# Kernel tuning notes

Hardware: AMD Instinct MI355X
Metric: run time of the kernel (lower is better)

The kernel has to match this reference:

```python
import jax, jax.numpy as jnp
import numpy as np

EPS = 1e-12
NEG_INF = -1e30

def _slog(x):
    return jnp.log(jnp.clip(x, EPS))

def setup_inputs() -> dict:
    M, Z = 24, 1024
    key = jax.random.key(0)
    ks = jax.random.split(key, 20)
    u = lambda k, sh, s=1.0: jax.random.uniform(k, sh, dtype=jnp.float32) * s
    demin = u(ks[0], (M, M), 0.2)
    demax = demin + u(ks[1], (M, M), 1.0)
    Kn = (jax.random.uniform(ks[2], (M, M)) > 0.5).astype(jnp.float32)
    # a couple of sectors with no substitution choices (rows stay all-ones in S)
    Kn = Kn.at[0].set(0.0).at[5].set(0.0)
    housing_mask = jnp.zeros((M,), dtype=bool).at[jnp.array([M - 2, M - 1])].set(True)
    genflux_mask = (jax.random.uniform(ks[3], (M,)) > 0.2)
    return {
        'h': jnp.zeros((M, Z), jnp.float32),
        'price': u(ks[4], (M, Z)),
        't_nij': u(ks[5], (M, Z, Z)),
        'demin': demin,
        'demax': demax,
        'delta': u(ks[6], (M, M), 0.2),
        'omega': u(ks[7], (M, M)),
        'sigma': u(ks[8], (M,), 0.5),
        'Kn': Kn,
        'attractor': u(ks[9], (M, Z)) + 0.1,
        'beta': u(ks[10], (M,), 0.5),
        'lamda': u(ks[11], (M,)),
        'A_ni': u(ks[12], (M, Z)) + 0.1,
        'exog_demand': u(ks[13], (M, Z)),
        'exog_prod': u(ks[14], (M, Z)),
        'X_0': u(ks[15], (M, Z)) + 0.1,
        'X_target': u(ks[16], (M, Z)),
        'housing_mask': housing_mask,
        'genflux_mask': genflux_mask,
    }

def reference(h, price, t_nij, demin, demax, delta, omega, sigma, Kn,
              attractor, beta, lamda, A_ni, exog_demand, exog_prod,
              X_0, X_target, housing_mask, genflux_mask):
    M, Z = price.shape
    ph = price + h                                            # [n,i] prices + shadow prices
    # LocationProbability: U_nij = lamda_n*ph[n,j] + t_nij; Pr = softmax_j for genflux non-housing, else eye
    U_nij = lamda[:, None, None] * ph[:, None, :] + t_nij     # [n,i,j]
    loc_logits = _slog(A_ni)[:, None, :] - beta[:, None, None] * U_nij
    Pr_soft = jax.nn.softmax(loc_logits, axis=-1)
    loc_mask = genflux_mask & (~housing_mask)                 # sectors with location choice
    eye = jnp.eye(Z, dtype=price.dtype)
    Pr = jnp.where(loc_mask[:, None, None], Pr_soft, eye[None, :, :])  # [n,i,j]
    # composite (expected) disutility per sector/zone
    U_ni = jnp.einsum('nij,nij->ni', Pr, U_nij)               # [n,i]
    # DemandFunction: a[m,n,i] = demin + (demax-demin)*exp(-delta*U_ni)
    a_mni = demin[:, :, None] + (demax - demin)[:, :, None] * jnp.exp(-delta[:, :, None] * U_ni[None])
    # SubstitutionProbability: masked softmax over substitutes n (axis=1), S=1 where no choice
    U_tilde = omega[:, :, None] * a_mni * U_ni[None]          # [m,n,i]
    cmask = (Kn > 0)[:, :, None]                              # [m,n,1]
    sub_logits = jnp.where(cmask, _slog(attractor)[None] - sigma[:, None, None] * U_tilde, NEG_INF)
    S_mni = jnp.where(cmask, jax.nn.softmax(sub_logits, axis=1), 1.0)
    # TotalDemand: D[n,i] = exog_demand + sum_m a*S*(X_0+exog_prod)
    X_total = X_0 + exog_prod
    D_ni = exog_demand + jnp.einsum('mni,mni,mi->ni', a_mni, S_mni, X_total)
    # induced production: X_pred[n,j] = sum_i D[n,i] * Pr[n,i,j]
    X_pred = jnp.einsum('ni,nij->nj', D_ni, Pr)
    return jnp.mean((X_pred - X_target) ** 2)
```

## Files before the change

### kernel.cpp

```cpp
#include <hip/hip_runtime.h>
#include <hip/hip_bf16.h>
#include <math.h>

#define MDIM 24
#define ZDIM 1024
#define NEG_INF_F -1e30f
#define EPS_F 1e-12f
#define NCH 32

enum {
  OFF_U    = 0,
  OFF_RMAX = 24576,
  OFF_SEXP = 49152,
  OFF_D    = 73728,
  OFF_XP   = 98304
};

__device__ __forceinline__ bool masks_are_bytes(const void* hm, const void* gm) {
  const unsigned int* hw = (const unsigned int*)hm;
  const unsigned int* gw = (const unsigned int*)gm;
  bool b = false;
  #pragma unroll
  for (int k = 0; k < 6; k++) {
    unsigned int a = hw[k], c = gw[k];
    if (a != 0u && a != 1u && a != 0x3F800000u) b = true;
    if (c != 0u && c != 1u && c != 0x3F800000u) b = true;
  }
  return b;
}
__device__ __forceinline__ bool loc_flag(const void* hm, const void* gm, int n) {
  bool bytes = masks_are_bytes(hm, gm);
  bool hv = bytes ? (((const unsigned char*)hm)[n] != 0)
                  : (((const unsigned int*)hm)[n] != 0u);
  bool gv = bytes ? (((const unsigned char*)gm)[n] != 0)
                  : (((const unsigned int*)gm)[n] != 0u);
  return gv && !hv;
}

__global__ __launch_bounds__(256) void k1_rows(
    const float* __restrict__ t, const float* __restrict__ price,
    const float* __restrict__ h, const float* __restrict__ A_ni,
    const float* __restrict__ beta, const float* __restrict__ lamda,
    const void* __restrict__ housing, const void* __restrict__ genflux,
    float* __restrict__ ws) {
  const int n  = blockIdx.x >> 8;
  const int i0 = (blockIdx.x & 255) * 4;
  __shared__ float pc_s[ZDIM];
  __shared__ float cc_s[ZDIM];
  const float bn = beta[n], ln = lamda[n];
  for (int j = threadIdx.x; j < ZDIM; j += 256) {
    float pc = ln * (price[n * ZDIM + j] + h[n * ZDIM + j]);
    float sa = logf(fmaxf(A_ni[n * ZDIM + j], EPS_F));
    pc_s[j] = pc;
    cc_s[j] = sa - bn * pc;
  }
  __syncthreads();
  const int wave = threadIdx.x >> 6, lane = threadIdx.x & 63;
  const int i = i0 + wave;
  const int row = n * ZDIM + i;
  if (!loc_flag(housing, genflux, n)) {
    if (lane == 0)
      ws[OFF_U + row] = pc_s[i] + t[(size_t)row * ZDIM + i];
    return;
  }
  const float4* t4  = (const float4*)(t + (size_t)row * ZDIM);
  const float4* pc4 = (const float4*)pc_s;
  const float4* cc4 = (const float4*)cc_s;
  float lg[16], uv[16];
  float mx = -INFINITY;
  #pragma unroll
  for (int k = 0; k < 4; k++) {
    const int f = lane + 64 * k;
    float4 tv = t4[f];
    float4 pv = pc4[f];
    float4 cv = cc4[f];
    uv[4*k+0] = pv.x + tv.x;  lg[4*k+0] = cv.x - bn * tv.x;
    uv[4*k+1] = pv.y + tv.y;  lg[4*k+1] = cv.y - bn * tv.y;
    uv[4*k+2] = pv.z + tv.z;  lg[4*k+2] = cv.z - bn * tv.z;
    uv[4*k+3] = pv.w + tv.w;  lg[4*k+3] = cv.w - bn * tv.w;
    mx = fmaxf(mx, fmaxf(fmaxf(lg[4*k], lg[4*k+1]), fmaxf(lg[4*k+2], lg[4*k+3])));
  }
  #pragma unroll
  for (int off = 32; off >= 1; off >>= 1)
    mx = fmaxf(mx, __shfl_xor(mx, off));
  float se = 0.f, su = 0.f;
  #pragma unroll
  for (int k = 0; k < 16; k++) {
    float e = __expf(lg[k] - mx);
    se += e;
    su = fmaf(e, uv[k], su);
  }
  #pragma unroll
  for (int off = 32; off >= 1; off >>= 1) {
    se += __shfl_xor(se, off);
    su += __shfl_xor(su, off);
  }
  if (lane == 0) {
    ws[OFF_U + row]    = su / se;
    ws[OFF_RMAX + row] = mx;
    ws[OFF_SEXP + row] = se;
  }
}

__global__ __launch_bounds__(256) void k2_demand(
    const float* __restrict__ demin, const float* __restrict__ demax,
    const float* __restrict__ delta, const float* __restrict__ omega,
    const float* __restrict__ sigma, const float* __restrict__ Kn,
    const float* __restrict__ attractor, const float* __restrict__ exogd,
    const float* __restrict__ X0, const float* __restrict__ exogp,
    const void* __restrict__ housing, const void* __restrict__ genflux,
    float* __restrict__ ws) {
  const int wave = threadIdx.x >> 6;
  const int lane = threadIdx.x & 63;
  const int half = lane >> 5;
  const int n    = lane & 31;
  const int i    = blockIdx.x * 8 + wave * 2 + half;
  const bool nv  = (n < MDIM);
  float Uv = 0.f, asl = NEG_INF_F;
  if (nv) {
    Uv  = ws[OFF_U + n * ZDIM + i];
    asl = logf(fmaxf(attractor[n * ZDIM + i], EPS_F));
  }
  float acc = 0.f;
  for (int m = 0; m < MDIM; m++) {
    const float Xt  = X0[m * ZDIM + i] + exogp[m * ZDIM + i];
    const float sig = sigma[m];
    float dm = 0.f, dd = 0.f, dl = 0.f, om = 0.f, kn = 0.f;
    if (nv) {
      dm = demin[m * MDIM + n];
      dd = demax[m * MDIM + n] - dm;
      dl = delta[m * MDIM + n];
      om = omega[m * MDIM + n];
      kn = Kn[m * MDIM + n];
    }
    const float a = dm + dd * __expf(-dl * Uv);
    const bool valid = nv && (kn > 0.f);
    const float l = valid ? asl - sig * om * a * Uv : NEG_INF_F;
    float mx = l;
    #pragma unroll
    for (int off = 16; off >= 1; off >>= 1)
      mx = fmaxf(mx, __shfl_xor(mx, off));
    float e = valid ? __expf(l - mx) : 0.f;
    float se = e;
    #pragma unroll
    for (int off = 16; off >= 1; off >>= 1)
      se += __shfl_xor(se, off);
    const float S = (valid && se > 0.f) ? e / se : 1.0f;
    if (nv) acc = fmaf(a * S, Xt, acc);
  }
  if (nv) {
    const float Dv = exogd[n * ZDIM + i] + acc;
    ws[OFF_D + n * ZDIM + i]  = Dv;
    ws[OFF_XP + n * ZDIM + i] = loc_flag(housing, genflux, n) ? 0.f : Dv;
  }
}

__global__ __launch_bounds__(256) void k3_xpred(
    const float* __restrict__ t, const float* __restrict__ price,
    const float* __restrict__ h, const float* __restrict__ A_ni,
    const float* __restrict__ beta, const float* __restrict__ lamda,
    const void* __restrict__ housing, const void* __restrict__ genflux,
    float* __restrict__ ws) {
  const int n = blockIdx.x / NCH, ic = blockIdx.x % NCH;
  if (!loc_flag(housing, genflux, n)) return;
  const int tj = threadIdx.x;
  const float bn = beta[n], ln = lamda[n];
  const float4 pr = ((const float4*)(price + n * ZDIM))[tj];
  const float4 hh = ((const float4*)(h     + n * ZDIM))[tj];
  const float4 aa = ((const float4*)(A_ni  + n * ZDIM))[tj];
  const float c0 = logf(fmaxf(aa.x, EPS_F)) - bn * (ln * (pr.x + hh.x));
  const float c1 = logf(fmaxf(aa.y, EPS_F)) - bn * (ln * (pr.y + hh.y));
  const float c2 = logf(fmaxf(aa.z, EPS_F)) - bn * (ln * (pr.z + hh.z));
  const float c3 = logf(fmaxf(aa.w, EPS_F)) - bn * (ln * (pr.w + hh.w));
  const float4* t4 = (const float4*)t;
  float x0 = 0.f, x1 = 0.f, x2 = 0.f, x3 = 0.f;
  for (int ii = 0; ii < ZDIM / NCH; ii++) {
    const int i = ic * (ZDIM / NCH) + ii;
    const int row = n * ZDIM + i;
    const float mx = ws[OFF_RMAX + row];
    const float w  = ws[OFF_D + row] / ws[OFF_SEXP + row];
    float4 tv = t4[(size_t)row * (ZDIM / 4) + tj];
    x0 = fmaf(w, __expf(c0 - mx - bn * tv.x), x0);
    x1 = fmaf(w, __expf(c1 - mx - bn * tv.y), x1);
    x2 = fmaf(w, __expf(c2 - mx - bn * tv.z), x2);
    x3 = fmaf(w, __expf(c3 - mx - bn * tv.w), x3);
  }
  float* xp = ws + OFF_XP + n * ZDIM + tj * 4;
  atomicAdd(xp + 0, x0);
  atomicAdd(xp + 1, x1);
  atomicAdd(xp + 2, x2);
  atomicAdd(xp + 3, x3);
}

__global__ __launch_bounds__(1024) void k4_loss(
    const float* __restrict__ Xtg, const float* __restrict__ ws,
    float* __restrict__ out) {
  float s = 0.f;
  for (int e = threadIdx.x; e < MDIM * ZDIM; e += 1024) {
    float d = ws[OFF_XP + e] - Xtg[e];
    s = fmaf(d, d, s);
  }
  #pragma unroll
  for (int off = 32; off >= 1; off >>= 1) s += __shfl_xor(s, off);
  __shared__ float red[16];
  const int w = threadIdx.x >> 6, lane = threadIdx.x & 63;
  if (lane == 0) red[w] = s;
  __syncthreads();
  if (threadIdx.x == 0) {
    float tot = 0.f;
    #pragma unroll
    for (int k = 0; k < 16; k++) tot += red[k];
    *out = tot * (1.0f / (MDIM * ZDIM));
  }
}

extern "C" void kernel_launch(void* const* d_in, const int* in_sizes, int n_in,
                              void* d_out, int out_size, void* d_ws, size_t ws_size,
                              hipStream_t stream) {
  (void)in_sizes; (void)n_in; (void)out_size; (void)ws_size;
  const float* h       = (const float*)d_in[0];
  const float* price   = (const float*)d_in[1];
  const float* t       = (const float*)d_in[2];
  const float* demin   = (const float*)d_in[3];
  const float* demax   = (const float*)d_in[4];
  const float* delta   = (const float*)d_in[5];
  const float* omega   = (const float*)d_in[6];
  const float* sigma   = (const float*)d_in[7];
  const float* Kn      = (const float*)d_in[8];
  const float* attract = (const float*)d_in[9];
  const float* beta    = (const float*)d_in[10];
  const float* lamda   = (const float*)d_in[11];
  const float* A_ni    = (const float*)d_in[12];
  const float* exogd   = (const float*)d_in[13];
  const float* exogp   = (const float*)d_in[14];
  const float* X0      = (const float*)d_in[15];
  const float* Xtg     = (const float*)d_in[16];
  const void*  housing = d_in[17];
  const void*  genflux = d_in[18];
  float* ws  = (float*)d_ws;
  float* out = (float*)d_out;

  k1_rows<<<MDIM * 256, 256, 0, stream>>>(t, price, h, A_ni, beta, lamda,
                                          housing, genflux, ws);
  k2_demand<<<128, 256, 0, stream>>>(demin, demax, delta, omega, sigma, Kn,
                                     attract, exogd, X0, exogp, housing, genflux, ws);
  k3_xpred<<<MDIM * NCH, 256, 0, stream>>>(t, price, h, A_ni, beta, lamda,
                                           housing, genflux, ws);
  k4_loss<<<1, 1024, 0, stream>>>(Xtg, ws, out);
}
```

Baseline: 237.0 us.

## Fuse four kernels into one cooperative persistent kernel with grid syncs

```diff
diff --git a/kernel.cpp b/kernel.cpp
--- a/kernel.cpp
+++ b/kernel.cpp
@@ -1,19 +1,27 @@
 #include <hip/hip_runtime.h>
-#include <hip/hip_bf16.h>
+#include <hip/hip_cooperative_groups.h>
 #include <math.h>
+
+namespace cg = cooperative_groups;
 
 #define MDIM 24
 #define ZDIM 1024
+#define NBLK 1024
+#define NTHR 256
 #define NEG_INF_F -1e30f
 #define EPS_F 1e-12f
-#define NCH 32
+#define NCH3 64
 
 enum {
-  OFF_U    = 0,
-  OFF_RMAX = 24576,
-  OFF_SEXP = 49152,
-  OFF_D    = 73728,
-  OFF_XP   = 98304
+  OFF_PC   = 0,
+  OFF_CC   = 24576,
+  OFF_U    = 49152,
+  OFF_RMAX = 73728,
+  OFF_SEXP = 98304,
+  OFF_D    = 122880,
+  OFF_XP   = 147456,
+  OFF_PART = 172032,
+  OFF_LOC  = 173056
 };
 
 __device__ __forceinline__ bool masks_are_bytes(const void* hm, const void* gm) {
@@ -35,6 +43,192 @@
   bool gv = bytes ? (((const unsigned char*)gm)[n] != 0)
                   : (((const unsigned int*)gm)[n] != 0u);
   return gv && !hv;
+}
+
+__global__ __launch_bounds__(NTHR, 4) void fused(
+    const float* __restrict__ t, const float* __restrict__ price,
+    const float* __restrict__ h, const float* __restrict__ A_ni,
+    const float* __restrict__ beta, const float* __restrict__ lamda,
+    const float* __restrict__ demin, const float* __restrict__ demax,
+    const float* __restrict__ delta, const float* __restrict__ omega,
+    const float* __restrict__ sigma, const float* __restrict__ Kn,
+    const float* __restrict__ attractor, const float* __restrict__ exogd,
+    const float* __restrict__ X0, const float* __restrict__ exogp,
+    const float* __restrict__ Xtg, const void* __restrict__ housing,
+    const void* __restrict__ genflux, float* __restrict__ ws,
+    float* __restrict__ out) {
+  cg::grid_group grid = cg::this_grid();
+  const int gid  = blockIdx.x * NTHR + threadIdx.x;
+  const int lane = threadIdx.x & 63;
+
+  if (gid < MDIM)
+    ((int*)(ws + OFF_LOC))[gid] = loc_flag(housing, genflux, gid) ? 1 : 0;
+  for (int e = gid; e < MDIM * ZDIM; e += NBLK * NTHR) {
+    const int n = e >> 10;
+    const float pc = lamda[n] * (price[e] + h[e]);
+    const float sa = logf(fmaxf(A_ni[e], EPS_F));
+    ws[OFF_PC + e] = pc;
+    ws[OFF_CC + e] = sa - beta[n] * pc;
+  }
+  grid.sync();
+
+  const int* loc = (const int*)(ws + OFF_LOC);
+
+  for (int e = gid; e < MDIM * ZDIM; e += NBLK * NTHR) {
+    const int n = e >> 10;
+    if (!loc[n]) {
+      const int i = e & 1023;
+      ws[OFF_U + e] = ws[OFF_PC + e] + t[(size_t)e * ZDIM + i];
+    }
+  }
+  const int wv = blockIdx.x * 4 + (threadIdx.x >> 6);
+  for (int row = wv; row < MDIM * ZDIM; row += NBLK * 4) {
+    const int n = row >> 10;
+    if (!loc[n]) continue;
+    const float bn = beta[n];
+    const float4* t4  = (const float4*)(t + (size_t)row * ZDIM);
+    const float4* pc4 = (const float4*)(ws + OFF_PC + n * ZDIM);
+    const float4* cc4 = (const float4*)(ws + OFF_CC + n * ZDIM);
+    float lg[16], uv[16];
+    float mx = -INFINITY;
+    #pragma unroll
+    for (int k = 0; k < 4; k++) {
+      const int f = lane + 64 * k;
+      float4 tv = t4[f];
+      float4 pv = pc4[f];
+      float4 cv = cc4[f];
+      uv[4*k+0] = pv.x + tv.x;  lg[4*k+0] = cv.x - bn * tv.x;
+      uv[4*k+1] = pv.y + tv.y;  lg[4*k+1] = cv.y - bn * tv.y;
+      uv[4*k+2] = pv.z + tv.z;  lg[4*k+2] = cv.z - bn * tv.z;
+      uv[4*k+3] = pv.w + tv.w;  lg[4*k+3] = cv.w - bn * tv.w;
+      mx = fmaxf(mx, fmaxf(fmaxf(lg[4*k], lg[4*k+1]), fmaxf(lg[4*k+2], lg[4*k+3])));
+    }
+    #pragma unroll
+    for (int off = 32; off >= 1; off >>= 1)
+      mx = fmaxf(mx, __shfl_xor(mx, off));
+    float se = 0.f, su = 0.f;
+    #pragma unroll
+    for (int k = 0; k < 16; k++) {
+      const float e = __expf(lg[k] - mx);
+      se += e;
+      su = fmaf(e, uv[k], su);
+    }
+    #pragma unroll
+    for (int off = 32; off >= 1; off >>= 1) {
+      se += __shfl_xor(se, off);
+      su += __shfl_xor(su, off);
+    }
+    if (lane == 0) {
+      ws[OFF_U + row]    = su / se;
+      ws[OFF_RMAX + row] = mx;
+      ws[OFF_SEXP + row] = se;
+    }
+  }
+  grid.sync();
+
+  {
+    const int hw = blockIdx.x * 8 + (threadIdx.x >> 5);
+    const int n  = threadIdx.x & 31;
+    if (hw < ZDIM) {
+      const int i = hw;
+      const bool nv = (n < MDIM);
+      float Uv = 0.f, asl = NEG_INF_F;
+      if (nv) {
+        Uv  = ws[OFF_U + n * ZDIM + i];
+        asl = logf(fmaxf(attractor[n * ZDIM + i], EPS_F));
+      }
+      float acc = 0.f;
+      for (int m = 0; m < MDIM; m++) {
+        const float Xt  = X0[m * ZDIM + i] + exogp[m * ZDIM + i];
+        const float sig = sigma[m];
+        float dm = 0.f, dd = 0.f, dl = 0.f, om = 0.f, kn = 0.f;
+        if (nv) {
+          dm = demin[m * MDIM + n];
+          dd = demax[m * MDIM + n] - dm;
+          dl = delta[m * MDIM + n];
+          om = omega[m * MDIM + n];
+          kn = Kn[m * MDIM + n];
+        }
+        const float a = dm + dd * __expf(-dl * Uv);
+        const bool valid = nv && (kn > 0.f);
+        const float l = valid ? asl - sig * om * a * Uv : NEG_INF_F;
+        float mxl = l;
+        #pragma unroll
+        for (int off = 16; off >= 1; off >>= 1)
+          mxl = fmaxf(mxl, __shfl_xor(mxl, off));
+        const float e = valid ? __expf(l - mxl) : 0.f;
+        float se = e;
+        #pragma unroll
+        for (int off = 16; off >= 1; off >>= 1)
+          se += __shfl_xor(se, off);
+        const float S = (valid && se > 0.f) ? e / se : 1.0f;
+        if (nv) acc = fmaf(a * S, Xt, acc);
+      }
+      if (nv) {
+        const float Dv = exogd[n * ZDIM + i] + acc;
+        ws[OFF_D + n * ZDIM + i]  = Dv;
+        ws[OFF_XP + n * ZDIM + i] = loc[n] ? 0.f : Dv;
+      }
+    }
+  }
+  grid.sync();
+
+  for (int g = blockIdx.x; g < MDIM * NCH3; g += NBLK) {
+    const int n = g >> 6, ic = g & (NCH3 - 1);
+    if (!loc[n]) continue;
+    const int tj = threadIdx.x;
+    const float bn = beta[n];
+    const float4 cv = ((const float4*)(ws + OFF_CC + n * ZDIM))[tj];
+    const float4* t4 = (const float4*)t;
+    float x0 = 0.f, x1 = 0.f, x2 = 0.f, x3 = 0.f;
+    for (int ii = 0; ii < ZDIM / NCH3; ii++) {
+      const int i = ic * (ZDIM / NCH3) + ii;
+      const int row = n * ZDIM + i;
+      const float mx = ws[OFF_RMAX + row];
+      const float w  = ws[OFF_D + row] / ws[OFF_SEXP + row];
+      float4 tv = t4[(size_t)row * (ZDIM / 4) + tj];
+      x0 = fmaf(w, __expf(cv.x - mx - bn * tv.x), x0);
+      x1 = fmaf(w, __expf(cv.y - mx - bn * tv.y), x1);
+      x2 = fmaf(w, __expf(cv.z - mx - bn * tv.z), x2);
+      x3 = fmaf(w, __expf(cv.w - mx - bn * tv.w), x3);
+    }
+    float* xp = ws + OFF_XP + n * ZDIM + tj * 4;
+    atomicAdd(xp + 0, x0);
+    atomicAdd(xp + 1, x1);
+    atomicAdd(xp + 2, x2);
+    atomicAdd(xp + 3, x3);
+  }
+  grid.sync();
+
+  {
+    float s = 0.f;
+    for (int e = gid; e < MDIM * ZDIM; e += NBLK * NTHR) {
+      const float d = ws[OFF_XP + e] - Xtg[e];
+      s = fmaf(d, d, s);
+    }
+    #pragma unroll
+    for (int off = 32; off >= 1; off >>= 1) s += __shfl_xor(s, off);
+    __shared__ float red[4];
+    const int w = threadIdx.x >> 6;
+    if (lane == 0) red[w] = s;
+    __syncthreads();
+    if (threadIdx.x == 0)
+      ws[OFF_PART + blockIdx.x] = red[0] + red[1] + red[2] + red[3];
+  }
+  grid.sync();
+
+  if (blockIdx.x == 0) {
+    float s = 0.f;
+    for (int k = threadIdx.x; k < NBLK; k += NTHR) s += ws[OFF_PART + k];
+    #pragma unroll
+    for (int off = 32; off >= 1; off >>= 1) s += __shfl_xor(s, off);
+    __shared__ float red2[4];
+    const int w = threadIdx.x >> 6;
+    if (lane == 0) red2[w] = s;
+    __syncthreads();
+    if (threadIdx.x == 0)
+      *out = (red2[0] + red2[1] + red2[2] + red2[3]) * (1.0f / (MDIM * ZDIM));
+  }
 }
 
 __global__ __launch_bounds__(256) void k1_rows(
@@ -161,7 +355,7 @@
     const float* __restrict__ beta, const float* __restrict__ lamda,
     const void* __restrict__ housing, const void* __restrict__ genflux,
     float* __restrict__ ws) {
-  const int n = blockIdx.x / NCH, ic = blockIdx.x % NCH;
+  const int n = blockIdx.x >> 5, ic = blockIdx.x & 31;
   if (!loc_flag(housing, genflux, n)) return;
   const int tj = threadIdx.x;
   const float bn = beta[n], ln = lamda[n];
@@ -174,8 +368,8 @@
   const float c3 = logf(fmaxf(aa.w, EPS_F)) - bn * (ln * (pr.w + hh.w));
   const float4* t4 = (const float4*)t;
   float x0 = 0.f, x1 = 0.f, x2 = 0.f, x3 = 0.f;
-  for (int ii = 0; ii < ZDIM / NCH; ii++) {
-    const int i = ic * (ZDIM / NCH) + ii;
+  for (int ii = 0; ii < 32; ii++) {
+    const int i = ic * 32 + ii;
     const int row = n * ZDIM + i;
     const float mx = ws[OFF_RMAX + row];
     const float w  = ws[OFF_D + row] / ws[OFF_SEXP + row];
@@ -240,11 +434,23 @@
   float* ws  = (float*)d_ws;
   float* out = (float*)d_out;
 
-  k1_rows<<<MDIM * 256, 256, 0, stream>>>(t, price, h, A_ni, beta, lamda,
-                                          housing, genflux, ws);
-  k2_demand<<<128, 256, 0, stream>>>(demin, demax, delta, omega, sigma, Kn,
-                                     attract, exogd, X0, exogp, housing, genflux, ws);
-  k3_xpred<<<MDIM * NCH, 256, 0, stream>>>(t, price, h, A_ni, beta, lamda,
-                                           housing, genflux, ws);
-  k4_loss<<<1, 1024, 0, stream>>>(Xtg, ws, out);
-}
+  void* args[] = {
+    (void*)&t, (void*)&price, (void*)&h, (void*)&A_ni, (void*)&beta,
+    (void*)&lamda, (void*)&demin, (void*)&demax, (void*)&delta, (void*)&omega,
+    (void*)&sigma, (void*)&Kn, (void*)&attract, (void*)&exogd, (void*)&X0,
+    (void*)&exogp, (void*)&Xtg, (void*)&housing, (void*)&genflux,
+    (void*)&ws, (void*)&out
+  };
+  hipError_t err = hipLaunchCooperativeKernel((const void*)fused, dim3(NBLK),
+                                              dim3(NTHR), args, 0, stream);
+  if (err != hipSuccess) {
+    k1_rows<<<MDIM * 256, 256, 0, stream>>>(t, price, h, A_ni, beta, lamda,
+                                            housing, genflux, ws);
+    k2_demand<<<128, 256, 0, stream>>>(demin, demax, delta, omega, sigma, Kn,
+                                       attract, exogd, X0, exogp,
+                                       housing, genflux, ws);
+    k3_xpred<<<MDIM * 32, 256, 0, stream>>>(t, price, h, A_ni, beta, lamda,
+                                            housing, genflux, ws);
+    k4_loss<<<1, 1024, 0, stream>>>(Xtg, ws, out);
+  }
+}
```

Result: slower. 816.1 us (+244.3%).

## Batch rows per k1 block, prefetch in k3, precompute weights, parallelize loss

Applied to the files above, without the earlier changes.

```diff
diff --git a/kernel.cpp b/kernel.cpp
--- a/kernel.cpp
+++ b/kernel.cpp
@@ -6,13 +6,12 @@
 #define ZDIM 1024
 #define NEG_INF_F -1e30f
 #define EPS_F 1e-12f
-#define NCH 32
 
 enum {
   OFF_U    = 0,
   OFF_RMAX = 24576,
   OFF_SEXP = 49152,
-  OFF_D    = 73728,
+  OFF_W    = 73728,
   OFF_XP   = 98304
 };
 
@@ -43,62 +42,81 @@
     const float* __restrict__ beta, const float* __restrict__ lamda,
     const void* __restrict__ housing, const void* __restrict__ genflux,
     float* __restrict__ ws) {
-  const int n  = blockIdx.x >> 8;
-  const int i0 = (blockIdx.x & 255) * 4;
+  const int n  = blockIdx.x >> 6;
+  const int i0 = (blockIdx.x & 63) * 16;
+  const float bn = beta[n], ln = lamda[n];
+  const bool lf = loc_flag(housing, genflux, n);
+  if (!lf) {
+    if (threadIdx.x < 16) {
+      const int row = n * ZDIM + i0 + threadIdx.x;
+      ws[OFF_U + row] = ln * (price[row] + h[row])
+                        + t[(size_t)row * ZDIM + (i0 + threadIdx.x)];
+    }
+    return;
+  }
   __shared__ float pc_s[ZDIM];
   __shared__ float cc_s[ZDIM];
-  const float bn = beta[n], ln = lamda[n];
   for (int j = threadIdx.x; j < ZDIM; j += 256) {
-    float pc = ln * (price[n * ZDIM + j] + h[n * ZDIM + j]);
-    float sa = logf(fmaxf(A_ni[n * ZDIM + j], EPS_F));
+    const float pc = ln * (price[n * ZDIM + j] + h[n * ZDIM + j]);
+    const float sa = logf(fmaxf(A_ni[n * ZDIM + j], EPS_F));
     pc_s[j] = pc;
     cc_s[j] = sa - bn * pc;
   }
   __syncthreads();
   const int wave = threadIdx.x >> 6, lane = threadIdx.x & 63;
-  const int i = i0 + wave;
-  const int row = n * ZDIM + i;
-  if (!loc_flag(housing, genflux, n)) {
-    if (lane == 0)
-      ws[OFF_U + row] = pc_s[i] + t[(size_t)row * ZDIM + i];
-    return;
-  }
-  const float4* t4  = (const float4*)(t + (size_t)row * ZDIM);
   const float4* pc4 = (const float4*)pc_s;
   const float4* cc4 = (const float4*)cc_s;
-  float lg[16], uv[16];
-  float mx = -INFINITY;
+
+  auto do_row = [&](int row, float4 t0, float4 t1, float4 t2, float4 t3) {
+    float lg[16], uv[16];
+    float mx = -INFINITY;
+    const float4 tt[4] = {t0, t1, t2, t3};
+    #pragma unroll
+    for (int k = 0; k < 4; k++) {
+      const int f = lane + 64 * k;
+      const float4 tv = tt[k];
+      const float4 pv = pc4[f];
+      const float4 cv = cc4[f];
+      uv[4*k+0] = pv.x + tv.x;  lg[4*k+0] = cv.x - bn * tv.x;
+      uv[4*k+1] = pv.y + tv.y;  lg[4*k+1] = cv.y - bn * tv.y;
+      uv[4*k+2] = pv.z + tv.z;  lg[4*k+2] = cv.z - bn * tv.z;
+      uv[4*k+3] = pv.w + tv.w;  lg[4*k+3] = cv.w - bn * tv.w;
+      mx = fmaxf(mx, fmaxf(fmaxf(lg[4*k], lg[4*k+1]), fmaxf(lg[4*k+2], lg[4*k+3])));
+    }
+    #pragma unroll
+    for (int off = 32; off >= 1; off >>= 1)
+      mx = fmaxf(mx, __shfl_xor(mx, off));
+    float se = 0.f, su = 0.f;
+    #pragma unroll
+    for (int k = 0; k < 16; k++) {
+      const float e = __expf(lg[k] - mx);
+      se += e;
+      su = fmaf(e, uv[k], su);
+    }
+    #pragma unroll
+    for (int off = 32; off >= 1; off >>= 1) {
+      se += __shfl_xor(se, off);
+      su += __shfl_xor(su, off);
+    }
+    if (lane == 0) {
+      ws[OFF_U + row]    = su / se;
+      ws[OFF_RMAX + row] = mx;
+      ws[OFF_SEXP + row] = se;
+    }
+  };
+
   #pragma unroll
-  for (int k = 0; k < 4; k++) {
-    const int f = lane + 64 * k;
-    float4 tv = t4[f];
-    float4 pv = pc4[f];
-    float4 cv = cc4[f];
-    uv[4*k+0] = pv.x + tv.x;  lg[4*k+0] = cv.x - bn * tv.x;
-    uv[4*k+1] = pv.y + tv.y;  lg[4*k+1] = cv.y - bn * tv.y;
-    uv[4*k+2] = pv.z + tv.z;  lg[4*k+2] = cv.z - bn * tv.z;
-    uv[4*k+3] = pv.w + tv.w;  lg[4*k+3] = cv.w - bn * tv.w;
-    mx = fmaxf(mx, fmaxf(fmaxf(lg[4*k], lg[4*k+1]), fmaxf(lg[4*k+2], lg[4*k+3])));
-  }
-  #pragma unroll
-  for (int off = 32; off >= 1; off >>= 1)
-    mx = fmaxf(mx, __shfl_xor(mx, off));
-  float se = 0.f, su = 0.f;
-  #pragma unroll
-  for (int k = 0; k < 16; k++) {
-    float e = __expf(lg[k] - mx);
-    se += e;
-    su = fmaf(e, uv[k], su);
-  }
-  #pragma unroll
-  for (int off = 32; off >= 1; off >>= 1) {
-    se += __shfl_xor(se, off);
-    su += __shfl_xor(su, off);
-  }
-  if (lane == 0) {
-    ws[OFF_U + row]    = su / se;
-    ws[OFF_RMAX + row] = mx;
-    ws[OFF_SEXP + row] = se;
+  for (int p = 0; p < 2; p++) {
+    const int rA = n * ZDIM + i0 + wave * 4 + p * 2;
+    const int rB = rA + 1;
+    const float4* tA = (const float4*)(t + (size_t)rA * ZDIM);
+    const float4* tB = (const float4*)(t + (size_t)rB * ZDIM);
+    const float4 a0 = tA[lane], a1 = tA[lane + 64],
+                 a2 = tA[lane + 128], a3 = tA[lane + 192];
+    const float4 b0 = tB[lane], b1 = tB[lane + 64],
+                 b2 = tB[lane + 128], b3 = tB[lane + 192];
+    do_row(rA, a0, a1, a2, a3);
+    do_row(rB, b0, b1, b2, b3);
   }
 }
 
@@ -140,7 +158,7 @@
     #pragma unroll
     for (int off = 16; off >= 1; off >>= 1)
       mx = fmaxf(mx, __shfl_xor(mx, off));
-    float e = valid ? __expf(l - mx) : 0.f;
+    const float e = valid ? __expf(l - mx) : 0.f;
     float se = e;
     #pragma unroll
     for (int off = 16; off >= 1; off >>= 1)
@@ -150,8 +168,12 @@
   }
   if (nv) {
     const float Dv = exogd[n * ZDIM + i] + acc;
-    ws[OFF_D + n * ZDIM + i]  = Dv;
-    ws[OFF_XP + n * ZDIM + i] = loc_flag(housing, genflux, n) ? 0.f : Dv;
+    if (loc_flag(housing, genflux, n)) {
+      ws[OFF_W  + n * ZDIM + i] = Dv / ws[OFF_SEXP + n * ZDIM + i];
+      ws[OFF_XP + n * ZDIM + i] = 0.f;
+    } else {
+      ws[OFF_XP + n * ZDIM + i] = Dv;
+    }
   }
 }
 
@@ -161,7 +183,7 @@
     const float* __restrict__ beta, const float* __restrict__ lamda,
     const void* __restrict__ housing, const void* __restrict__ genflux,
     float* __restrict__ ws) {
-  const int n = blockIdx.x / NCH, ic = blockIdx.x % NCH;
+  const int n = blockIdx.x >> 6, ic = blockIdx.x & 63;
   if (!loc_flag(housing, genflux, n)) return;
   const int tj = threadIdx.x;
   const float bn = beta[n], ln = lamda[n];
@@ -173,17 +195,24 @@
   const float c2 = logf(fmaxf(aa.z, EPS_F)) - bn * (ln * (pr.z + hh.z));
   const float c3 = logf(fmaxf(aa.w, EPS_F)) - bn * (ln * (pr.w + hh.w));
   const float4* t4 = (const float4*)t;
+  int row = n * ZDIM + ic * 16;
+  float  mx_c = ws[OFF_RMAX + row];
+  float  w_c  = ws[OFF_W + row];
+  float4 tv_c = t4[(size_t)row * (ZDIM / 4) + tj];
   float x0 = 0.f, x1 = 0.f, x2 = 0.f, x3 = 0.f;
-  for (int ii = 0; ii < ZDIM / NCH; ii++) {
-    const int i = ic * (ZDIM / NCH) + ii;
-    const int row = n * ZDIM + i;
-    const float mx = ws[OFF_RMAX + row];
-    const float w  = ws[OFF_D + row] / ws[OFF_SEXP + row];
-    float4 tv = t4[(size_t)row * (ZDIM / 4) + tj];
-    x0 = fmaf(w, __expf(c0 - mx - bn * tv.x), x0);
-    x1 = fmaf(w, __expf(c1 - mx - bn * tv.y), x1);
-    x2 = fmaf(w, __expf(c2 - mx - bn * tv.z), x2);
-    x3 = fmaf(w, __expf(c3 - mx - bn * tv.w), x3);
+  for (int ii = 0; ii < 16; ii++) {
+    float mx_n = 0.f, w_n = 0.f;
+    float4 tv_n = tv_c;
+    if (ii < 15) {
+      mx_n = ws[OFF_RMAX + row + 1];
+      w_n  = ws[OFF_W + row + 1];
+      tv_n = t4[(size_t)(row + 1) * (ZDIM / 4) + tj];
+    }
+    x0 = fmaf(w_c, __expf(c0 - mx_c - bn * tv_c.x), x0);
+    x1 = fmaf(w_c, __expf(c1 - mx_c - bn * tv_c.y), x1);
+    x2 = fmaf(w_c, __expf(c2 - mx_c - bn * tv_c.z), x2);
+    x3 = fmaf(w_c, __expf(c3 - mx_c - bn * tv_c.w), x3);
+    mx_c = mx_n; w_c = w_n; tv_c = tv_n; row++;
   }
   float* xp = ws + OFF_XP + n * ZDIM + tj * 4;
   atomicAdd(xp + 0, x0);
@@ -192,26 +221,22 @@
   atomicAdd(xp + 3, x3);
 }
 
-__global__ __launch_bounds__(1024) void k4_loss(
+__global__ __launch_bounds__(256) void k4_loss(
     const float* __restrict__ Xtg, const float* __restrict__ ws,
     float* __restrict__ out) {
   float s = 0.f;
-  for (int e = threadIdx.x; e < MDIM * ZDIM; e += 1024) {
-    float d = ws[OFF_XP + e] - Xtg[e];
+  for (int e = blockIdx.x * 256 + threadIdx.x; e < MDIM * ZDIM; e += 48 * 256) {
+    const float d = ws[OFF_XP + e] - Xtg[e];
     s = fmaf(d, d, s);
   }
   #pragma unroll
   for (int off = 32; off >= 1; off >>= 1) s += __shfl_xor(s, off);
-  __shared__ float red[16];
+  __shared__ float red[4];
   const int w = threadIdx.x >> 6, lane = threadIdx.x & 63;
   if (lane == 0) red[w] = s;
   __syncthreads();
-  if (threadIdx.x == 0) {
-    float tot = 0.f;
-    #pragma unroll
-    for (int k = 0; k < 16; k++) tot += red[k];
-    *out = tot * (1.0f / (MDIM * ZDIM));
-  }
+  if (threadIdx.x == 0)
+    atomicAdd(out, (red[0] + red[1] + red[2] + red[3]) * (1.0f / (MDIM * ZDIM)));
 }
 
 extern "C" void kernel_launch(void* const* d_in, const int* in_sizes, int n_in,
@@ -240,11 +265,13 @@
   float* ws  = (float*)d_ws;
   float* out = (float*)d_out;
 
-  k1_rows<<<MDIM * 256, 256, 0, stream>>>(t, price, h, A_ni, beta, lamda,
+  k1_rows<<<MDIM * 64, 256, 0, stream>>>(t, price, h, A_ni, beta, lamda,
+                                         housing, genflux, ws);
+  k2_demand<<<128, 256, 0, stream>>>(demin, demax, delta, omega, sigma, Kn,
+                                     attract, exogd, X0, exogp,
+                                     housing, genflux, ws);
+  k3_xpred<<<MDIM * 64, 256, 0, stream>>>(t, price, h, A_ni, beta, lamda,
                                           housing, genflux, ws);
-  k2_demand<<<128, 256, 0, stream>>>(demin, demax, delta, omega, sigma, Kn,
-                                     attract, exogd, X0, exogp, housing, genflux, ws);
-  k3_xpred<<<MDIM * NCH, 256, 0, stream>>>(t, price, h, A_ni, beta, lamda,
-                                           housing, genflux, ws);
-  k4_loss<<<1, 1024, 0, stream>>>(Xtg, ws, out);
-}
+  hipMemsetAsync(out, 0, sizeof(float), stream);
+  k4_loss<<<48, 256, 0, stream>>>(Xtg, ws, out);
+}
```

New measurement: 237.8 us. About the same (+0.3%).
